# Kernel optimization log

Hardware: AMD Instinct MI355X
Metric: run time of the kernel (lower is better)

The kernel has to match this reference:

```python
import jax, jax.numpy as jnp
import numpy as np

D = 1024
H = 16
HD = D // H
SCALE = HD ** -0.5


def setup_inputs() -> dict:
    key = jax.random.key(0)
    ks = jax.random.split(key, 5)
    x = jax.random.normal(ks[0], (2, 2048, D), dtype=jnp.float32)
    s = 1.0 / np.sqrt(D)
    W_qkv = jax.random.uniform(ks[1], (D, 3 * D), jnp.float32, -s, s)
    b_qkv = jax.random.uniform(ks[2], (3 * D,), jnp.float32, -s, s)
    W_out = jax.random.uniform(ks[3], (D, D), jnp.float32, -s, s)
    b_out = jax.random.uniform(ks[4], (D,), jnp.float32, -s, s)
    return {"x": x, "W_qkv": W_qkv, "b_qkv": b_qkv, "W_out": W_out, "b_out": b_out}


def reference(x, W_qkv, b_qkv, W_out, b_out):
    B, S, _ = x.shape
    qkv = x @ W_qkv + b_qkv                       # [B,S,3D]
    qkv = qkv.reshape(B, S, 3, H, HD)
    q, k, v = jnp.moveaxis(qkv, 2, 0)             # each [B,S,H,HD]
    # scores: [B,H,S,S]
    scores = jnp.einsum("bshd,bthd->bhst", q, k) * SCALE
    attn = jax.nn.softmax(scores, axis=-1)        # dropout is identity in eval mode
    out = jnp.einsum("bhst,bthd->bshd", attn, v)  # [B,S,H,HD]
    out = out.reshape(B, S, H * HD)
    return out @ W_out + b_out
```

## Files before the change

### kernel.cpp

```cpp
#include <hip/hip_runtime.h>

typedef unsigned short u16;
typedef unsigned int   u32;

using short8 = __attribute__((ext_vector_type(8))) short;
using f32x4  = __attribute__((ext_vector_type(4))) float;
using half4  = __attribute__((ext_vector_type(4))) _Float16;
using half8  = __attribute__((ext_vector_type(8))) _Float16;

#define QSCALE 0.18033688011112042f

__device__ __forceinline__ u16 f2bf(float f) {
  u32 u = __float_as_uint(f);
  return (u16)((u + 0x8000u) >> 16);
}
__device__ __forceinline__ u16 f2h(float f) {
  _Float16 h = (_Float16)f;
  return __builtin_bit_cast(u16, h);
}

__device__ __forceinline__ void gld16(const u16* g, u16* l) {
  __builtin_amdgcn_global_load_lds(
      (const __attribute__((address_space(1))) unsigned int*)g,
      (__attribute__((address_space(3))) unsigned int*)l, 16, 0, 0);
}

__global__ __launch_bounds__(256) void cvt_x(const float* __restrict__ in,
                                             u16* __restrict__ out) {
  int idx = blockIdx.x * 256 + threadIdx.x;
  float4 v = reinterpret_cast<const float4*>(in)[idx];
  ushort4 o;
  o.x = f2bf(v.x); o.y = f2bf(v.y); o.z = f2bf(v.z); o.w = f2bf(v.w);
  reinterpret_cast<ushort4*>(out)[idx] = o;
}

__global__ __launch_bounds__(256) void transpose_w(const float* __restrict__ in,
                                                   u16* __restrict__ out,
                                                   int R, int C) {
  __shared__ u32 s[32][33];
  int c0 = blockIdx.x * 32, r0 = blockIdx.y * 32;
  int j = threadIdx.x & 31, i0 = threadIdx.x >> 5;
#pragma unroll
  for (int p = 0; p < 4; ++p) {
    int i = i0 + p * 8;
    s[i][j] = f2bf(in[(size_t)(r0 + i) * C + c0 + j]);
  }
  __syncthreads();
#pragma unroll
  for (int p = 0; p < 4; ++p) {
    int jj = i0 + p * 8;
    out[(size_t)(c0 + jj) * R + r0 + j] = (u16)s[j][jj];
  }
}

__global__ __launch_bounds__(256, 2) void gemm_qkv(
    const u16* __restrict__ A, const u16* __restrict__ Bt,
    const float* __restrict__ bias,
    u16* __restrict__ q_out, u16* __restrict__ k_out, u16* __restrict__ vt_out) {
  const int K = 1024;
  __shared__ __align__(16) u16 As[4][128 * 32];
  __shared__ __align__(16) u16 Bs[4][192 * 32];
  const int tid = threadIdx.x;
  const int lane = tid & 63, wv = tid >> 6;
  const int l16 = lane & 15, quad = lane >> 4;
  const int wm = wv & 1, wn = wv >> 1;
  const int bx = blockIdx.x, by = blockIdx.y;

  const u16* Ab = A + (size_t)by * 128 * K;
  const u16* Bb = Bt + (size_t)bx * 192 * K;

  const int iA0 = tid, iA1 = 256 + tid;
  const int iB0 = tid, iB1 = 256 + tid, iB2 = 512 + tid;
  const u16* sA0 = Ab + (size_t)(iA0 >> 2) * K + (((iA0 & 3) ^ ((iA0 >> 2) & 3)) << 3);
  const u16* sA1 = Ab + (size_t)(iA1 >> 2) * K + (((iA1 & 3) ^ ((iA1 >> 2) & 3)) << 3);
  const u16* sB0 = Bb + (size_t)(iB0 >> 2) * K + (((iB0 & 3) ^ ((iB0 >> 2) & 3)) << 3);
  const u16* sB1 = Bb + (size_t)(iB1 >> 2) * K + (((iB1 & 3) ^ ((iB1 >> 2) & 3)) << 3);
  const u16* sB2 = Bb + (size_t)(iB2 >> 2) * K + (((iB2 & 3) ^ ((iB2 >> 2) & 3)) << 3);
  const int dA0 = iA0 << 3, dA1 = iA1 << 3;
  const int dB0 = iB0 << 3, dB1 = iB1 << 3, dB2 = iB2 << 3;

  int aoff[4], boff[6];
#pragma unroll
  for (int mi = 0; mi < 4; ++mi) {
    int r = wm * 64 + mi * 16 + l16;
    aoff[mi] = r * 32 + ((quad ^ (r & 3)) << 3);
  }
#pragma unroll
  for (int ni = 0; ni < 6; ++ni) {
    int r = wn * 96 + ni * 16 + l16;
    boff[ni] = r * 32 + ((quad ^ (r & 3)) << 3);
  }

  const f32x4 fzero = {0.0f, 0.0f, 0.0f, 0.0f};
  f32x4 acc[4][6];
#pragma unroll
  for (int i = 0; i < 4; ++i)
#pragma unroll
    for (int j = 0; j < 6; ++j) acc[i][j] = fzero;

#define STAGE_A(T)                        \
  do {                                    \
    gld16(sA0, &As[T][dA0]);              \
    gld16(sA1, &As[T][dA1]);              \
    sA0 += 32; sA1 += 32;                 \
  } while (0)
#define STAGE_B(T)                        \
  do {                                    \
    gld16(sB0, &Bs[T][dB0]);              \
    gld16(sB1, &Bs[T][dB1]);              \
    gld16(sB2, &Bs[T][dB2]);              \
    sB0 += 32; sB1 += 32; sB2 += 32;      \
  } while (0)
#define VM5 asm volatile("s_waitcnt vmcnt(5)" ::: "memory")
#define VM0 asm volatile("s_waitcnt vmcnt(0)" ::: "memory")

#define GTILE(S, T, DOST, VW)                                              \
  do {                                                                     \
    short8 bb[6];                                                          \
    _Pragma("unroll")                                                      \
    for (int j = 0; j < 6; ++j)                                            \
      bb[j] = *reinterpret_cast<const short8*>(&Bs[S][boff[j]]);           \
    short8 a0 = *reinterpret_cast<const short8*>(&As[S][aoff[0]]);         \
    short8 a1 = *reinterpret_cast<const short8*>(&As[S][aoff[1]]);         \
    if (DOST) { STAGE_A(T); }                                              \
    __builtin_amdgcn_s_barrier();                                          \
    __builtin_amdgcn_s_setprio(1);                                         \
    _Pragma("unroll")                                                      \
    for (int j = 0; j < 6; ++j) {                                          \
      acc[0][j] = __builtin_amdgcn_mfma_f32_16x16x32_bf16(a0, bb[j], acc[0][j], 0, 0, 0); \
      acc[1][j] = __builtin_amdgcn_mfma_f32_16x16x32_bf16(a1, bb[j], acc[1][j], 0, 0, 0); \
    }                                                                      \
    __builtin_amdgcn_s_setprio(0);                                         \
    __builtin_amdgcn_s_barrier();                                          \
    short8 a2 = *reinterpret_cast<const short8*>(&As[S][aoff[2]]);         \
    short8 a3 = *reinterpret_cast<const short8*>(&As[S][aoff[3]]);         \
    if (DOST) { STAGE_B(T); }                                              \
    __builtin_amdgcn_s_barrier();                                          \
    __builtin_amdgcn_s_setprio(1);                                         \
    _Pragma("unroll")                                                      \
    for (int j = 0; j < 6; ++j) {                                          \
      acc[2][j] = __builtin_amdgcn_mfma_f32_16x16x32_bf16(a2, bb[j], acc[2][j], 0, 0, 0); \
      acc[3][j] = __builtin_amdgcn_mfma_f32_16x16x32_bf16(a3, bb[j], acc[3][j], 0, 0, 0); \
    }                                                                      \
    __builtin_amdgcn_s_setprio(0);                                         \
    VW;                                                                    \
    __builtin_amdgcn_s_barrier();                                          \
  } while (0)

  STAGE_A(0); STAGE_B(0);
  STAGE_A(1); STAGE_B(1);
  VM5;
  __builtin_amdgcn_s_barrier();

  for (int kb = 0; kb < 28; kb += 4) {
    GTILE(0, 2, 1, VM5);
    GTILE(1, 3, 1, VM5);
    GTILE(2, 0, 1, VM5);
    GTILE(3, 1, 1, VM5);
  }
  GTILE(0, 2, 1, VM5);
  GTILE(1, 3, 1, VM5);
  GTILE(2, 0, 0, VM0);
  GTILE(3, 1, 0, ((void)0));
#undef GTILE
#undef STAGE_A
#undef STAGE_B

#pragma unroll
  for (int mi = 0; mi < 4; ++mi)
#pragma unroll
    for (int ni = 0; ni < 6; ++ni) {
      int col = bx * 192 + wn * 96 + ni * 16 + l16;
      float bv = bias[col];
      int row0 = by * 128 + wm * 64 + mi * 16 + quad * 4;
      int which = col >> 10, rem = col & 1023;
      int h = rem >> 6, d = rem & 63;
      int b = row0 >> 11, sq0 = row0 & 2047;
      int bh = (b << 4) + h;
      if (which == 2) {
        ushort4 pk;
        pk.x = f2h(acc[mi][ni][0] + bv);
        pk.y = f2h(acc[mi][ni][1] + bv);
        pk.z = f2h(acc[mi][ni][2] + bv);
        pk.w = f2h(acc[mi][ni][3] + bv);
        size_t off = (size_t)bh * 131072 +
                     (((sq0 >> 2) * 16 + (d & 15)) * 16 + ((d >> 4) << 2));
        *reinterpret_cast<ushort4*>(&vt_out[off]) = pk;
      } else {
        size_t base = (size_t)(bh * 2048 + sq0) * 64 + d;
#pragma unroll
        for (int r = 0; r < 4; ++r) {
          float val = acc[mi][ni][r] + bv;
          if (which == 0) q_out[base + r * 64] = f2bf(val * QSCALE);
          else            k_out[base + r * 64] = f2bf(val);
        }
      }
    }
}

template <int EPI, int MT>
__global__ __launch_bounds__(256, 3) void gemm_bt(
    const u16* __restrict__ A, const u16* __restrict__ Bt,
    const float* __restrict__ bias, float* __restrict__ c_out,
    u16* __restrict__ q_out, u16* __restrict__ k_out, u16* __restrict__ vt_out,
    int M, int N, int K) {
  __shared__ __align__(16) u16 As[32 * MT * 32];
  __shared__ __align__(16) u16 Bs[128 * 32];
  const int tid = threadIdx.x;
  const int lane = tid & 63;
  const int wv = tid >> 6;
  const int l16 = lane & 15, quad = lane >> 4;
  const int wm = wv & 1, wn = wv >> 1;
  const int bx = blockIdx.x, by = blockIdx.y;

  const u16* Ab = A + (size_t)by * (32 * MT) * K;
  const u16* Bb = Bt + (size_t)bx * 128 * K;

  const f32x4 fzero = {0.0f, 0.0f, 0.0f, 0.0f};
  f32x4 acc[MT][4];
#pragma unroll
  for (int i = 0; i < MT; ++i)
#pragma unroll
    for (int j = 0; j < 4; ++j) acc[i][j] = fzero;

  for (int k0 = 0; k0 < K; k0 += 32) {
    __syncthreads();
#pragma unroll
    for (int p = 0; p < MT / 2; ++p) {
      int id = p * 256 + tid;
      int row = id >> 2, blk = id & 3;
      int gc = k0 + ((blk ^ (row & 3)) << 3);
      gld16(Ab + (size_t)row * K + gc, &As[id << 3]);
    }
#pragma unroll
    for (int p = 0; p < 2; ++p) {
      int id = p * 256 + tid;
      int row = id >> 2, blk = id & 3;
      int gc = k0 + ((blk ^ (row & 3)) << 3);
      gld16(Bb + (size_t)row * K + gc, &Bs[id << 3]);
    }
    __syncthreads();
    short8 af[MT], bfr[4];
#pragma unroll
    for (int mi = 0; mi < MT; ++mi) {
      int row = wm * (MT * 16) + mi * 16 + l16;
      af[mi] = *reinterpret_cast<const short8*>(&As[row * 32 + ((quad ^ (row & 3)) << 3)]);
    }
#pragma unroll
    for (int ni = 0; ni < 4; ++ni) {
      int row = wn * 64 + ni * 16 + l16;
      bfr[ni] = *reinterpret_cast<const short8*>(&Bs[row * 32 + ((quad ^ (row & 3)) << 3)]);
    }
#pragma unroll
    for (int mi = 0; mi < MT; ++mi)
#pragma unroll
      for (int ni = 0; ni < 4; ++ni)
        acc[mi][ni] = __builtin_amdgcn_mfma_f32_16x16x32_bf16(af[mi], bfr[ni], acc[mi][ni], 0, 0, 0);
  }

#pragma unroll
  for (int mi = 0; mi < MT; ++mi)
#pragma unroll
    for (int ni = 0; ni < 4; ++ni) {
      int col = bx * 128 + wn * 64 + ni * 16 + l16;
      float bv = bias[col];
      int row0 = by * (32 * MT) + wm * (MT * 16) + mi * 16 + quad * 4;
      if (EPI == 1) {
#pragma unroll
        for (int r = 0; r < 4; ++r)
          c_out[(size_t)(row0 + r) * N + col] = acc[mi][ni][r] + bv;
      } else {
        int which = col >> 10, rem = col & 1023;
        int h = rem >> 6, d = rem & 63;
        int b = row0 >> 11, sq0 = row0 & 2047;
        int bh = (b << 4) + h;
        if (which == 2) {
          ushort4 pk;
          pk.x = f2h(acc[mi][ni][0] + bv);
          pk.y = f2h(acc[mi][ni][1] + bv);
          pk.z = f2h(acc[mi][ni][2] + bv);
          pk.w = f2h(acc[mi][ni][3] + bv);
          size_t off = (size_t)bh * 131072 +
                       (((sq0 >> 2) * 16 + (d & 15)) * 16 + ((d >> 4) << 2));
          *reinterpret_cast<ushort4*>(&vt_out[off]) = pk;
        } else {
          size_t base = (size_t)(bh * 2048 + sq0) * 64 + d;
#pragma unroll
          for (int r = 0; r < 4; ++r) {
            float val = acc[mi][ni][r] + bv;
            if (which == 0) q_out[base + r * 64] = f2bf(val * QSCALE);
            else            k_out[base + r * 64] = f2bf(val);
          }
        }
      }
    }
}

__global__ __launch_bounds__(256, 4) void attn(
    const u16* __restrict__ q_buf, const u16* __restrict__ k_buf,
    const u16* __restrict__ vt_buf, u16* __restrict__ o_buf) {
  __shared__ __align__(16) u16 Ks[2][4096];
  __shared__ __align__(16) u16 Vs[2][4096];

  const int tid = threadIdx.x;
  const int lane = tid & 63, w = tid >> 6;
  const int l16 = lane & 15, quad = lane >> 4;
  const int bh = blockIdx.x, q0 = blockIdx.y * 64;

  const u16* qg = q_buf + (size_t)bh * 131072 + (q0 + w * 16) * 64;
  const u16* kg = k_buf + (size_t)bh * 131072;
  const u16* vg = vt_buf + (size_t)bh * 131072;

  short8 qb[2];
#pragma unroll
  for (int kk = 0; kk < 2; ++kk)
    qb[kk] = *reinterpret_cast<const short8*>(qg + l16 * 64 + kk * 32 + quad * 8);

  const int idA = tid, idB = 256 + tid;
  const u16* ksA = kg + (idA >> 3) * 64 + (((idA & 7) ^ ((idA >> 3) & 7)) << 3);
  const u16* ksB = kg + (idB >> 3) * 64 + (((idB & 7) ^ ((idB >> 3) & 7)) << 3);
  const u16* vsA = vg + ((idA ^ ((idA >> 4) & 1)) << 3);
  const u16* vsB = vg + ((idB ^ ((idB >> 4) & 1)) << 3);
  const int ldA = idA << 3, ldB = idB << 3;

  int k0o[4], k1o[4], v0o[4], v1o[4];
#pragma unroll
  for (int t = 0; t < 4; ++t) {
    int rr = t * 16 + l16;
    k0o[t] = rr * 64 + ((quad ^ (rr & 7)) << 3);
    k1o[t] = rr * 64 + (((4 + quad) ^ (rr & 7)) << 3);
    int gb = (t * 4 + quad) * 32 + l16 * 2;
    int sw = (l16 >> 3) & 1;
    v0o[t] = (gb + sw) << 3;
    v1o[t] = (gb + (sw ^ 1)) << 3;
  }

  const f32x4 fzero = {0.0f, 0.0f, 0.0f, 0.0f};
  f32x4 o_acc[4];
  float l_acc = 0.f;
#pragma unroll
  for (int nd = 0; nd < 4; ++nd) o_acc[nd] = fzero;

#define STAGE(BUF)                           \
  do {                                       \
    gld16(ksA, &Ks[BUF][ldA]);               \
    gld16(ksB, &Ks[BUF][ldB]);               \
    gld16(vsA, &Vs[BUF][ldA]);               \
    gld16(vsB, &Vs[BUF][ldB]);               \
    ksA += 4096; ksB += 4096;                \
    vsA += 4096; vsB += 4096;                \
  } while (0)

#define TILE(BUF)                                                         \
  do {                                                                    \
    _Pragma("unroll")                                                     \
    for (int t = 0; t < 4; ++t) {                                         \
      short8 k0f = *reinterpret_cast<const short8*>(&Ks[BUF][k0o[t]]);    \
      short8 k1f = *reinterpret_cast<const short8*>(&Ks[BUF][k1o[t]]);    \
      half8 v0 = *reinterpret_cast<const half8*>(&Vs[BUF][v0o[t]]);       \
      half8 v1 = *reinterpret_cast<const half8*>(&Vs[BUF][v1o[t]]);       \
      half4 vb0 = __builtin_shufflevector(v0, v0, 0, 1, 2, 3);            \
      half4 vb1 = __builtin_shufflevector(v0, v0, 4, 5, 6, 7);            \
      half4 vb2 = __builtin_shufflevector(v1, v1, 0, 1, 2, 3);            \
      half4 vb3 = __builtin_shufflevector(v1, v1, 4, 5, 6, 7);            \
      __builtin_amdgcn_s_setprio(1);                                      \
      f32x4 s = __builtin_amdgcn_mfma_f32_16x16x32_bf16(k0f, qb[0], fzero, 0, 0, 0); \
      s = __builtin_amdgcn_mfma_f32_16x16x32_bf16(k1f, qb[1], s, 0, 0, 0);\
      __builtin_amdgcn_s_setprio(0);                                      \
      float p0 = __builtin_amdgcn_exp2f(s[0]);                            \
      float p1 = __builtin_amdgcn_exp2f(s[1]);                            \
      float p2 = __builtin_amdgcn_exp2f(s[2]);                            \
      float p3 = __builtin_amdgcn_exp2f(s[3]);                            \
      l_acc += (p0 + p1) + (p2 + p3);                                     \
      half4 pa;                                                           \
      pa[0] = (_Float16)p0; pa[1] = (_Float16)p1;                         \
      pa[2] = (_Float16)p2; pa[3] = (_Float16)p3;                         \
      __builtin_amdgcn_s_setprio(1);                                      \
      o_acc[0] = __builtin_amdgcn_mfma_f32_16x16x16f16(pa, vb0, o_acc[0], 0, 0, 0); \
      o_acc[1] = __builtin_amdgcn_mfma_f32_16x16x16f16(pa, vb1, o_acc[1], 0, 0, 0); \
      o_acc[2] = __builtin_amdgcn_mfma_f32_16x16x16f16(pa, vb2, o_acc[2], 0, 0, 0); \
      o_acc[3] = __builtin_amdgcn_mfma_f32_16x16x16f16(pa, vb3, o_acc[3], 0, 0, 0); \
      __builtin_amdgcn_s_setprio(0);                                      \
    }                                                                     \
  } while (0)

  STAGE(0);
  __syncthreads();

  for (int i = 0; i < 32; i += 2) {
    if (i + 1 < 32) STAGE(1);
    TILE(0);
    __syncthreads();
    if (i + 2 < 32) STAGE(0);
    TILE(1);
    __syncthreads();
  }
#undef STAGE
#undef TILE

  l_acc += __shfl_xor(l_acc, 16, 64);
  l_acc += __shfl_xor(l_acc, 32, 64);

  const int b = bh >> 4, h = bh & 15;
  float lv[4];
#pragma unroll
  for (int r = 0; r < 4; ++r)
    lv[r] = __shfl(l_acc, quad * 4 + r, 64);
#pragma unroll
  for (int nd = 0; nd < 4; ++nd) {
#pragma unroll
    for (int r = 0; r < 4; ++r) {
      int sq = q0 + w * 16 + quad * 4 + r;
      o_buf[(size_t)(b * 2048 + sq) * 1024 + h * 64 + nd * 16 + l16] =
          f2bf(o_acc[nd][r] / lv[r]);
    }
  }
}

extern "C" void kernel_launch(void* const* d_in, const int* in_sizes, int n_in,
                              void* d_out, int out_size, void* d_ws, size_t ws_size,
                              hipStream_t stream) {
  (void)in_sizes; (void)n_in; (void)out_size; (void)ws_size;
  const float* x     = (const float*)d_in[0];
  const float* W_qkv = (const float*)d_in[1];
  const float* b_qkv = (const float*)d_in[2];
  const float* W_out = (const float*)d_in[3];
  const float* b_out = (const float*)d_in[4];
  float* out = (float*)d_out;

  char* ws = (char*)d_ws;
  u16* x_bf   = (u16*)(ws);
  u16* wqkv_t = (u16*)(ws + 8388608);
  u16* wout_t = (u16*)(ws + 14680064);
  u16* q_buf  = (u16*)(ws + 16777216);
  u16* k_buf  = (u16*)(ws + 25165824);
  u16* vt_buf = (u16*)(ws + 33554432);
  u16* o_bf   = (u16*)(ws + 41943040);

  cvt_x<<<4096, 256, 0, stream>>>(x, x_bf);
  transpose_w<<<dim3(96, 32), 256, 0, stream>>>(W_qkv, wqkv_t, 1024, 3072);
  transpose_w<<<dim3(32, 32), 256, 0, stream>>>(W_out, wout_t, 1024, 1024);
  gemm_qkv<<<dim3(16, 32), 256, 0, stream>>>(x_bf, wqkv_t, b_qkv,
                                             q_buf, k_buf, vt_buf);
  attn<<<dim3(32, 32), 256, 0, stream>>>(q_buf, k_buf, vt_buf, o_bf);
  gemm_bt<1, 2><<<dim3(8, 64), 256, 0, stream>>>(o_bf, wout_t, b_out, out,
                                                 nullptr, nullptr, nullptr, 4096, 1024, 1024);
}
```

Before: 188.3 us.

## Double per-wave query rows and use four-stage K/V pipeline in attention

Each wave in the attention kernel now handles 32 query rows instead of 16, so every K/V tile loaded into shared memory is reused for twice the MFMA work, and the grid is halved to match. K/V staging moves from a double buffer to a four-deep ring. Loads are issued inside the tile loop and waited on with explicit vmcnt counts and raw barriers in place of __syncthreads. The cost is more registers and LDS per block, and the launch bound drops occupancy from 4 to 2 blocks per CU, with half as many blocks to spread across CUs.

Measured after the change: 189.1 us. About the same (+0.4%).

```diff
diff --git a/kernel.cpp b/kernel.cpp
--- a/kernel.cpp
+++ b/kernel.cpp
@@ -296,25 +296,28 @@
     }
 }
 
-__global__ __launch_bounds__(256, 4) void attn(
+__global__ __launch_bounds__(256, 2) void attn(
     const u16* __restrict__ q_buf, const u16* __restrict__ k_buf,
     const u16* __restrict__ vt_buf, u16* __restrict__ o_buf) {
-  __shared__ __align__(16) u16 Ks[2][4096];
-  __shared__ __align__(16) u16 Vs[2][4096];
+  __shared__ __align__(16) u16 Ks[4][4096];
+  __shared__ __align__(16) u16 Vs[4][4096];
 
   const int tid = threadIdx.x;
   const int lane = tid & 63, w = tid >> 6;
   const int l16 = lane & 15, quad = lane >> 4;
-  const int bh = blockIdx.x, q0 = blockIdx.y * 64;
-
-  const u16* qg = q_buf + (size_t)bh * 131072 + (q0 + w * 16) * 64;
+  const int bh = blockIdx.x, q0 = blockIdx.y * 128;
+
+  const u16* qg = q_buf + (size_t)bh * 131072 + (q0 + w * 32) * 64;
   const u16* kg = k_buf + (size_t)bh * 131072;
   const u16* vg = vt_buf + (size_t)bh * 131072;
 
-  short8 qb[2];
-#pragma unroll
-  for (int kk = 0; kk < 2; ++kk)
-    qb[kk] = *reinterpret_cast<const short8*>(qg + l16 * 64 + kk * 32 + quad * 8);
+  short8 qb[2][2];
+#pragma unroll
+  for (int qi = 0; qi < 2; ++qi)
+#pragma unroll
+    for (int kk = 0; kk < 2; ++kk)
+      qb[qi][kk] = *reinterpret_cast<const short8*>(
+          qg + (qi * 16 + l16) * 64 + kk * 32 + quad * 8);
 
   const int idA = tid, idB = 256 + tid;
   const u16* ksA = kg + (idA >> 3) * 64 + (((idA & 7) ^ ((idA >> 3) & 7)) << 3);
@@ -336,83 +339,103 @@
   }
 
   const f32x4 fzero = {0.0f, 0.0f, 0.0f, 0.0f};
-  f32x4 o_acc[4];
-  float l_acc = 0.f;
-#pragma unroll
-  for (int nd = 0; nd < 4; ++nd) o_acc[nd] = fzero;
-
-#define STAGE(BUF)                           \
+  f32x4 o_acc[2][4];
+  float l_acc[2] = {0.f, 0.f};
+#pragma unroll
+  for (int qi = 0; qi < 2; ++qi)
+#pragma unroll
+    for (int nd = 0; nd < 4; ++nd) o_acc[qi][nd] = fzero;
+
+#define STAGE(T)                             \
   do {                                       \
-    gld16(ksA, &Ks[BUF][ldA]);               \
-    gld16(ksB, &Ks[BUF][ldB]);               \
-    gld16(vsA, &Vs[BUF][ldA]);               \
-    gld16(vsB, &Vs[BUF][ldB]);               \
+    gld16(ksA, &Ks[T][ldA]);                 \
+    gld16(ksB, &Ks[T][ldB]);                 \
+    gld16(vsA, &Vs[T][ldA]);                 \
+    gld16(vsB, &Vs[T][ldB]);                 \
     ksA += 4096; ksB += 4096;                \
     vsA += 4096; vsB += 4096;                \
   } while (0)
-
-#define TILE(BUF)                                                         \
+#define VM4 asm volatile("s_waitcnt vmcnt(4)" ::: "memory")
+#define VM0a asm volatile("s_waitcnt vmcnt(0)" ::: "memory")
+
+#define ATILE(S, T, DOST, VW)                                             \
   do {                                                                    \
     _Pragma("unroll")                                                     \
     for (int t = 0; t < 4; ++t) {                                         \
-      short8 k0f = *reinterpret_cast<const short8*>(&Ks[BUF][k0o[t]]);    \
-      short8 k1f = *reinterpret_cast<const short8*>(&Ks[BUF][k1o[t]]);    \
-      half8 v0 = *reinterpret_cast<const half8*>(&Vs[BUF][v0o[t]]);       \
-      half8 v1 = *reinterpret_cast<const half8*>(&Vs[BUF][v1o[t]]);       \
+      short8 k0f = *reinterpret_cast<const short8*>(&Ks[S][k0o[t]]);      \
+      short8 k1f = *reinterpret_cast<const short8*>(&Ks[S][k1o[t]]);      \
+      half8 v0 = *reinterpret_cast<const half8*>(&Vs[S][v0o[t]]);         \
+      half8 v1 = *reinterpret_cast<const half8*>(&Vs[S][v1o[t]]);         \
+      if (DOST && t == 0) STAGE(T);                                       \
       half4 vb0 = __builtin_shufflevector(v0, v0, 0, 1, 2, 3);            \
       half4 vb1 = __builtin_shufflevector(v0, v0, 4, 5, 6, 7);            \
       half4 vb2 = __builtin_shufflevector(v1, v1, 0, 1, 2, 3);            \
       half4 vb3 = __builtin_shufflevector(v1, v1, 4, 5, 6, 7);            \
-      __builtin_amdgcn_s_setprio(1);                                      \
-      f32x4 s = __builtin_amdgcn_mfma_f32_16x16x32_bf16(k0f, qb[0], fzero, 0, 0, 0); \
-      s = __builtin_amdgcn_mfma_f32_16x16x32_bf16(k1f, qb[1], s, 0, 0, 0);\
-      __builtin_amdgcn_s_setprio(0);                                      \
-      float p0 = __builtin_amdgcn_exp2f(s[0]);                            \
-      float p1 = __builtin_amdgcn_exp2f(s[1]);                            \
-      float p2 = __builtin_amdgcn_exp2f(s[2]);                            \
-      float p3 = __builtin_amdgcn_exp2f(s[3]);                            \
-      l_acc += (p0 + p1) + (p2 + p3);                                     \
-      half4 pa;                                                           \
-      pa[0] = (_Float16)p0; pa[1] = (_Float16)p1;                         \
-      pa[2] = (_Float16)p2; pa[3] = (_Float16)p3;                         \
-      __builtin_amdgcn_s_setprio(1);                                      \
-      o_acc[0] = __builtin_amdgcn_mfma_f32_16x16x16f16(pa, vb0, o_acc[0], 0, 0, 0); \
-      o_acc[1] = __builtin_amdgcn_mfma_f32_16x16x16f16(pa, vb1, o_acc[1], 0, 0, 0); \
-      o_acc[2] = __builtin_amdgcn_mfma_f32_16x16x16f16(pa, vb2, o_acc[2], 0, 0, 0); \
-      o_acc[3] = __builtin_amdgcn_mfma_f32_16x16x16f16(pa, vb3, o_acc[3], 0, 0, 0); \
-      __builtin_amdgcn_s_setprio(0);                                      \
+      _Pragma("unroll")                                                   \
+      for (int qi = 0; qi < 2; ++qi) {                                    \
+        __builtin_amdgcn_s_setprio(1);                                    \
+        f32x4 s = __builtin_amdgcn_mfma_f32_16x16x32_bf16(k0f, qb[qi][0], fzero, 0, 0, 0); \
+        s = __builtin_amdgcn_mfma_f32_16x16x32_bf16(k1f, qb[qi][1], s, 0, 0, 0); \
+        __builtin_amdgcn_s_setprio(0);                                    \
+        float p0 = __builtin_amdgcn_exp2f(s[0]);                          \
+        float p1 = __builtin_amdgcn_exp2f(s[1]);                          \
+        float p2 = __builtin_amdgcn_exp2f(s[2]);                          \
+        float p3 = __builtin_amdgcn_exp2f(s[3]);                          \
+        l_acc[qi] += (p0 + p1) + (p2 + p3);                               \
+        half4 pa;                                                         \
+        pa[0] = (_Float16)p0; pa[1] = (_Float16)p1;                       \
+        pa[2] = (_Float16)p2; pa[3] = (_Float16)p3;                       \
+        __builtin_amdgcn_s_setprio(1);                                    \
+        o_acc[qi][0] = __builtin_amdgcn_mfma_f32_16x16x16f16(pa, vb0, o_acc[qi][0], 0, 0, 0); \
+        o_acc[qi][1] = __builtin_amdgcn_mfma_f32_16x16x16f16(pa, vb1, o_acc[qi][1], 0, 0, 0); \
+        o_acc[qi][2] = __builtin_amdgcn_mfma_f32_16x16x16f16(pa, vb2, o_acc[qi][2], 0, 0, 0); \
+        o_acc[qi][3] = __builtin_amdgcn_mfma_f32_16x16x16f16(pa, vb3, o_acc[qi][3], 0, 0, 0); \
+        __builtin_amdgcn_s_setprio(0);                                    \
+      }                                                                   \
     }                                                                     \
+    VW;                                                                   \
+    __builtin_amdgcn_s_barrier();                                         \
   } while (0)
 
   STAGE(0);
-  __syncthreads();
-
-  for (int i = 0; i < 32; i += 2) {
-    if (i + 1 < 32) STAGE(1);
-    TILE(0);
-    __syncthreads();
-    if (i + 2 < 32) STAGE(0);
-    TILE(1);
-    __syncthreads();
-  }
+  STAGE(1);
+  VM4;
+  __builtin_amdgcn_s_barrier();
+
+  for (int i = 0; i < 28; i += 4) {
+    ATILE(0, 2, 1, VM4);
+    ATILE(1, 3, 1, VM4);
+    ATILE(2, 0, 1, VM4);
+    ATILE(3, 1, 1, VM4);
+  }
+  ATILE(0, 2, 1, VM4);
+  ATILE(1, 3, 1, VM4);
+  ATILE(2, 0, 0, VM0a);
+  ATILE(3, 0, 0, ((void)0));
+#undef ATILE
 #undef STAGE
-#undef TILE
-
-  l_acc += __shfl_xor(l_acc, 16, 64);
-  l_acc += __shfl_xor(l_acc, 32, 64);
+
+#pragma unroll
+  for (int qi = 0; qi < 2; ++qi) {
+    l_acc[qi] += __shfl_xor(l_acc[qi], 16, 64);
+    l_acc[qi] += __shfl_xor(l_acc[qi], 32, 64);
+  }
 
   const int b = bh >> 4, h = bh & 15;
-  float lv[4];
-#pragma unroll
-  for (int r = 0; r < 4; ++r)
-    lv[r] = __shfl(l_acc, quad * 4 + r, 64);
-#pragma unroll
-  for (int nd = 0; nd < 4; ++nd) {
-#pragma unroll
-    for (int r = 0; r < 4; ++r) {
-      int sq = q0 + w * 16 + quad * 4 + r;
-      o_buf[(size_t)(b * 2048 + sq) * 1024 + h * 64 + nd * 16 + l16] =
-          f2bf(o_acc[nd][r] / lv[r]);
+#pragma unroll
+  for (int qi = 0; qi < 2; ++qi) {
+    float lv[4];
+#pragma unroll
+    for (int r = 0; r < 4; ++r)
+      lv[r] = __shfl(l_acc[qi], quad * 4 + r, 64);
+#pragma unroll
+    for (int nd = 0; nd < 4; ++nd) {
+#pragma unroll
+      for (int r = 0; r < 4; ++r) {
+        int sq = q0 + w * 32 + qi * 16 + quad * 4 + r;
+        o_buf[(size_t)(b * 2048 + sq) * 1024 + h * 64 + nd * 16 + l16] =
+            f2bf(o_acc[qi][nd][r] / lv[r]);
+      }
     }
   }
 }
@@ -442,7 +465,7 @@
   transpose_w<<<dim3(32, 32), 256, 0, stream>>>(W_out, wout_t, 1024, 1024);
   gemm_qkv<<<dim3(16, 32), 256, 0, stream>>>(x_bf, wqkv_t, b_qkv,
                                              q_buf, k_buf, vt_buf);
-  attn<<<dim3(32, 32), 256, 0, stream>>>(q_buf, k_buf, vt_buf, o_bf);
+  attn<<<dim3(32, 16), 256, 0, stream>>>(q_buf, k_buf, vt_buf, o_bf);
   gemm_bt<1, 2><<<dim3(8, 64), 256, 0, stream>>>(o_bf, wout_t, b_out, out,
                                                  nullptr, nullptr, nullptr, 4096, 1024, 1024);
 }
```

## Merge prep kernels and pipeline output projection GEMM with 4-stage async loads

Applied to the files above, without the earlier changes.

Folds the x conversion and both weight transposes into one prep kernel, which removes two launches. Replaces the output-projection GEMM's single-buffered loop with a 4-stage global_load_lds pipeline modelled on the QKV GEMM, with interleaved barriers, setprio and partial vmcnt waits, on 128x64 tiles. It also changes the LDS XOR swizzle to mix in higher row bits, which is meant to reduce bank conflicts. The cost is more LDS per block and occupancy dropping from 3 to 2 blocks.

Result: faster. 184.3 us (-2.1%).

```diff
diff --git a/kernel.cpp b/kernel.cpp
--- a/kernel.cpp
+++ b/kernel.cpp
@@ -9,6 +9,7 @@
 using half8  = __attribute__((ext_vector_type(8))) _Float16;
 
 #define QSCALE 0.18033688011112042f
+#define SXR(r) ((((r) ^ ((r) >> 2))) & 3)
 
 __device__ __forceinline__ u16 f2bf(float f) {
   u32 u = __float_as_uint(f);
@@ -25,21 +26,25 @@
       (__attribute__((address_space(3))) unsigned int*)l, 16, 0, 0);
 }
 
-__global__ __launch_bounds__(256) void cvt_x(const float* __restrict__ in,
-                                             u16* __restrict__ out) {
-  int idx = blockIdx.x * 256 + threadIdx.x;
-  float4 v = reinterpret_cast<const float4*>(in)[idx];
-  ushort4 o;
-  o.x = f2bf(v.x); o.y = f2bf(v.y); o.z = f2bf(v.z); o.w = f2bf(v.w);
-  reinterpret_cast<ushort4*>(out)[idx] = o;
-}
-
-__global__ __launch_bounds__(256) void transpose_w(const float* __restrict__ in,
-                                                   u16* __restrict__ out,
-                                                   int R, int C) {
+__global__ __launch_bounds__(256) void prep(
+    const float* __restrict__ x, u16* __restrict__ x_bf,
+    const float* __restrict__ Wq, u16* __restrict__ wq_t,
+    const float* __restrict__ Wo, u16* __restrict__ wo_t) {
   __shared__ u32 s[32][33];
-  int c0 = blockIdx.x * 32, r0 = blockIdx.y * 32;
-  int j = threadIdx.x & 31, i0 = threadIdx.x >> 5;
+  const int bid = blockIdx.x, tid = threadIdx.x;
+  if (bid < 4096) {
+    int idx = bid * 256 + tid;
+    float4 v = reinterpret_cast<const float4*>(x)[idx];
+    ushort4 o;
+    o.x = f2bf(v.x); o.y = f2bf(v.y); o.z = f2bf(v.z); o.w = f2bf(v.w);
+    reinterpret_cast<ushort4*>(x_bf)[idx] = o;
+    return;
+  }
+  const float* in; u16* out; int R, C, bx, by;
+  if (bid < 7168) { int b = bid - 4096; in = Wq; out = wq_t; R = 1024; C = 3072; bx = b % 96; by = b / 96; }
+  else            { int b = bid - 7168; in = Wo; out = wo_t; R = 1024; C = 1024; bx = b % 32; by = b / 32; }
+  int c0 = bx * 32, r0 = by * 32;
+  int j = tid & 31, i0 = tid >> 5;
 #pragma unroll
   for (int p = 0; p < 4; ++p) {
     int i = i0 + p * 8;
@@ -71,11 +76,11 @@
 
   const int iA0 = tid, iA1 = 256 + tid;
   const int iB0 = tid, iB1 = 256 + tid, iB2 = 512 + tid;
-  const u16* sA0 = Ab + (size_t)(iA0 >> 2) * K + (((iA0 & 3) ^ ((iA0 >> 2) & 3)) << 3);
-  const u16* sA1 = Ab + (size_t)(iA1 >> 2) * K + (((iA1 & 3) ^ ((iA1 >> 2) & 3)) << 3);
-  const u16* sB0 = Bb + (size_t)(iB0 >> 2) * K + (((iB0 & 3) ^ ((iB0 >> 2) & 3)) << 3);
-  const u16* sB1 = Bb + (size_t)(iB1 >> 2) * K + (((iB1 & 3) ^ ((iB1 >> 2) & 3)) << 3);
-  const u16* sB2 = Bb + (size_t)(iB2 >> 2) * K + (((iB2 & 3) ^ ((iB2 >> 2) & 3)) << 3);
+  const u16* sA0 = Ab + (size_t)(iA0 >> 2) * K + (((iA0 & 3) ^ SXR(iA0 >> 2)) << 3);
+  const u16* sA1 = Ab + (size_t)(iA1 >> 2) * K + (((iA1 & 3) ^ SXR(iA1 >> 2)) << 3);
+  const u16* sB0 = Bb + (size_t)(iB0 >> 2) * K + (((iB0 & 3) ^ SXR(iB0 >> 2)) << 3);
+  const u16* sB1 = Bb + (size_t)(iB1 >> 2) * K + (((iB1 & 3) ^ SXR(iB1 >> 2)) << 3);
+  const u16* sB2 = Bb + (size_t)(iB2 >> 2) * K + (((iB2 & 3) ^ SXR(iB2 >> 2)) << 3);
   const int dA0 = iA0 << 3, dA1 = iA1 << 3;
   const int dB0 = iB0 << 3, dB1 = iB1 << 3, dB2 = iB2 << 3;
 
@@ -83,12 +88,12 @@
 #pragma unroll
   for (int mi = 0; mi < 4; ++mi) {
     int r = wm * 64 + mi * 16 + l16;
-    aoff[mi] = r * 32 + ((quad ^ (r & 3)) << 3);
+    aoff[mi] = r * 32 + ((quad ^ SXR(r)) << 3);
   }
 #pragma unroll
   for (int ni = 0; ni < 6; ++ni) {
     int r = wn * 96 + ni * 16 + l16;
-    boff[ni] = r * 32 + ((quad ^ (r & 3)) << 3);
+    boff[ni] = r * 32 + ((quad ^ SXR(r)) << 3);
   }
 
   const f32x4 fzero = {0.0f, 0.0f, 0.0f, 0.0f};
@@ -198,101 +203,118 @@
     }
 }
 
-template <int EPI, int MT>
-__global__ __launch_bounds__(256, 3) void gemm_bt(
+__global__ __launch_bounds__(256, 2) void gemm_op(
     const u16* __restrict__ A, const u16* __restrict__ Bt,
-    const float* __restrict__ bias, float* __restrict__ c_out,
-    u16* __restrict__ q_out, u16* __restrict__ k_out, u16* __restrict__ vt_out,
-    int M, int N, int K) {
-  __shared__ __align__(16) u16 As[32 * MT * 32];
-  __shared__ __align__(16) u16 Bs[128 * 32];
+    const float* __restrict__ bias, float* __restrict__ c_out) {
+  const int K = 1024;
+  __shared__ __align__(16) u16 As[4][128 * 32];
+  __shared__ __align__(16) u16 Bs[4][64 * 32];
   const int tid = threadIdx.x;
-  const int lane = tid & 63;
-  const int wv = tid >> 6;
+  const int lane = tid & 63, wv = tid >> 6;
   const int l16 = lane & 15, quad = lane >> 4;
   const int wm = wv & 1, wn = wv >> 1;
   const int bx = blockIdx.x, by = blockIdx.y;
 
-  const u16* Ab = A + (size_t)by * (32 * MT) * K;
-  const u16* Bb = Bt + (size_t)bx * 128 * K;
+  const u16* Ab = A + (size_t)by * 128 * K;
+  const u16* Bb = Bt + (size_t)bx * 64 * K;
+
+  const int iA0 = tid, iA1 = 256 + tid, iB0 = tid;
+  const u16* sA0 = Ab + (size_t)(iA0 >> 2) * K + (((iA0 & 3) ^ SXR(iA0 >> 2)) << 3);
+  const u16* sA1 = Ab + (size_t)(iA1 >> 2) * K + (((iA1 & 3) ^ SXR(iA1 >> 2)) << 3);
+  const u16* sB0 = Bb + (size_t)(iB0 >> 2) * K + (((iB0 & 3) ^ SXR(iB0 >> 2)) << 3);
+  const int dA0 = iA0 << 3, dA1 = iA1 << 3, dB0 = iB0 << 3;
+
+  int aoff[4], boff[2];
+#pragma unroll
+  for (int mi = 0; mi < 4; ++mi) {
+    int r = wm * 64 + mi * 16 + l16;
+    aoff[mi] = r * 32 + ((quad ^ SXR(r)) << 3);
+  }
+#pragma unroll
+  for (int ni = 0; ni < 2; ++ni) {
+    int r = wn * 32 + ni * 16 + l16;
+    boff[ni] = r * 32 + ((quad ^ SXR(r)) << 3);
+  }
 
   const f32x4 fzero = {0.0f, 0.0f, 0.0f, 0.0f};
-  f32x4 acc[MT][4];
-#pragma unroll
-  for (int i = 0; i < MT; ++i)
-#pragma unroll
-    for (int j = 0; j < 4; ++j) acc[i][j] = fzero;
-
-  for (int k0 = 0; k0 < K; k0 += 32) {
-    __syncthreads();
-#pragma unroll
-    for (int p = 0; p < MT / 2; ++p) {
-      int id = p * 256 + tid;
-      int row = id >> 2, blk = id & 3;
-      int gc = k0 + ((blk ^ (row & 3)) << 3);
-      gld16(Ab + (size_t)row * K + gc, &As[id << 3]);
-    }
-#pragma unroll
-    for (int p = 0; p < 2; ++p) {
-      int id = p * 256 + tid;
-      int row = id >> 2, blk = id & 3;
-      int gc = k0 + ((blk ^ (row & 3)) << 3);
-      gld16(Bb + (size_t)row * K + gc, &Bs[id << 3]);
-    }
-    __syncthreads();
-    short8 af[MT], bfr[4];
-#pragma unroll
-    for (int mi = 0; mi < MT; ++mi) {
-      int row = wm * (MT * 16) + mi * 16 + l16;
-      af[mi] = *reinterpret_cast<const short8*>(&As[row * 32 + ((quad ^ (row & 3)) << 3)]);
-    }
-#pragma unroll
-    for (int ni = 0; ni < 4; ++ni) {
-      int row = wn * 64 + ni * 16 + l16;
-      bfr[ni] = *reinterpret_cast<const short8*>(&Bs[row * 32 + ((quad ^ (row & 3)) << 3)]);
-    }
-#pragma unroll
-    for (int mi = 0; mi < MT; ++mi)
-#pragma unroll
-      for (int ni = 0; ni < 4; ++ni)
-        acc[mi][ni] = __builtin_amdgcn_mfma_f32_16x16x32_bf16(af[mi], bfr[ni], acc[mi][ni], 0, 0, 0);
-  }
-
-#pragma unroll
-  for (int mi = 0; mi < MT; ++mi)
-#pragma unroll
-    for (int ni = 0; ni < 4; ++ni) {
-      int col = bx * 128 + wn * 64 + ni * 16 + l16;
+  f32x4 acc[4][2];
+#pragma unroll
+  for (int i = 0; i < 4; ++i)
+#pragma unroll
+    for (int j = 0; j < 2; ++j) acc[i][j] = fzero;
+
+#define STAGE_A(T)                        \
+  do {                                    \
+    gld16(sA0, &As[T][dA0]);              \
+    gld16(sA1, &As[T][dA1]);              \
+    sA0 += 32; sA1 += 32;                 \
+  } while (0)
+#define STAGE_B(T)                        \
+  do {                                    \
+    gld16(sB0, &Bs[T][dB0]);              \
+    sB0 += 32;                            \
+  } while (0)
+#define VM3 asm volatile("s_waitcnt vmcnt(3)" ::: "memory")
+#define VM0b asm volatile("s_waitcnt vmcnt(0)" ::: "memory")
+
+#define OTILE(S, T, DOST, VW)                                              \
+  do {                                                                     \
+    short8 b0 = *reinterpret_cast<const short8*>(&Bs[S][boff[0]]);         \
+    short8 b1 = *reinterpret_cast<const short8*>(&Bs[S][boff[1]]);         \
+    short8 a0 = *reinterpret_cast<const short8*>(&As[S][aoff[0]]);         \
+    short8 a1 = *reinterpret_cast<const short8*>(&As[S][aoff[1]]);         \
+    if (DOST) { STAGE_A(T); }                                              \
+    __builtin_amdgcn_s_barrier();                                          \
+    __builtin_amdgcn_s_setprio(1);                                         \
+    acc[0][0] = __builtin_amdgcn_mfma_f32_16x16x32_bf16(a0, b0, acc[0][0], 0, 0, 0); \
+    acc[0][1] = __builtin_amdgcn_mfma_f32_16x16x32_bf16(a0, b1, acc[0][1], 0, 0, 0); \
+    acc[1][0] = __builtin_amdgcn_mfma_f32_16x16x32_bf16(a1, b0, acc[1][0], 0, 0, 0); \
+    acc[1][1] = __builtin_amdgcn_mfma_f32_16x16x32_bf16(a1, b1, acc[1][1], 0, 0, 0); \
+    __builtin_amdgcn_s_setprio(0);                                         \
+    __builtin_amdgcn_s_barrier();                                          \
+    short8 a2 = *reinterpret_cast<const short8*>(&As[S][aoff[2]]);         \
+    short8 a3 = *reinterpret_cast<const short8*>(&As[S][aoff[3]]);         \
+    if (DOST) { STAGE_B(T); }                                              \
+    __builtin_amdgcn_s_barrier();                                          \
+    __builtin_amdgcn_s_setprio(1);                                         \
+    acc[2][0] = __builtin_amdgcn_mfma_f32_16x16x32_bf16(a2, b0, acc[2][0], 0, 0, 0); \
+    acc[2][1] = __builtin_amdgcn_mfma_f32_16x16x32_bf16(a2, b1, acc[2][1], 0, 0, 0); \
+    acc[3][0] = __builtin_amdgcn_mfma_f32_16x16x32_bf16(a3, b0, acc[3][0], 0, 0, 0); \
+    acc[3][1] = __builtin_amdgcn_mfma_f32_16x16x32_bf16(a3, b1, acc[3][1], 0, 0, 0); \
+    __builtin_amdgcn_s_setprio(0);                                         \
+    VW;                                                                    \
+    __builtin_amdgcn_s_barrier();                                          \
+  } while (0)
+
+  STAGE_A(0); STAGE_B(0);
+  STAGE_A(1); STAGE_B(1);
+  VM3;
+  __builtin_amdgcn_s_barrier();
+
+  for (int kb = 0; kb < 28; kb += 4) {
+    OTILE(0, 2, 1, VM3);
+    OTILE(1, 3, 1, VM3);
+    OTILE(2, 0, 1, VM3);
+    OTILE(3, 1, 1, VM3);
+  }
+  OTILE(0, 2, 1, VM3);
+  OTILE(1, 3, 1, VM3);
+  OTILE(2, 0, 0, VM0b);
+  OTILE(3, 1, 0, ((void)0));
+#undef OTILE
+#undef STAGE_A
+#undef STAGE_B
+
+#pragma unroll
+  for (int mi = 0; mi < 4; ++mi)
+#pragma unroll
+    for (int ni = 0; ni < 2; ++ni) {
+      int col = bx * 64 + wn * 32 + ni * 16 + l16;
       float bv = bias[col];
-      int row0 = by * (32 * MT) + wm * (MT * 16) + mi * 16 + quad * 4;
-      if (EPI == 1) {
-#pragma unroll
-        for (int r = 0; r < 4; ++r)
-          c_out[(size_t)(row0 + r) * N + col] = acc[mi][ni][r] + bv;
-      } else {
-        int which = col >> 10, rem = col & 1023;
-        int h = rem >> 6, d = rem & 63;
-        int b = row0 >> 11, sq0 = row0 & 2047;
-        int bh = (b << 4) + h;
-        if (which == 2) {
-          ushort4 pk;
-          pk.x = f2h(acc[mi][ni][0] + bv);
-          pk.y = f2h(acc[mi][ni][1] + bv);
-          pk.z = f2h(acc[mi][ni][2] + bv);
-          pk.w = f2h(acc[mi][ni][3] + bv);
-          size_t off = (size_t)bh * 131072 +
-                       (((sq0 >> 2) * 16 + (d & 15)) * 16 + ((d >> 4) << 2));
-          *reinterpret_cast<ushort4*>(&vt_out[off]) = pk;
-        } else {
-          size_t base = (size_t)(bh * 2048 + sq0) * 64 + d;
-#pragma unroll
-          for (int r = 0; r < 4; ++r) {
-            float val = acc[mi][ni][r] + bv;
-            if (which == 0) q_out[base + r * 64] = f2bf(val * QSCALE);
-            else            k_out[base + r * 64] = f2bf(val);
-          }
-        }
-      }
+      int row0 = by * 128 + wm * 64 + mi * 16 + quad * 4;
+#pragma unroll
+      for (int r = 0; r < 4; ++r)
+        c_out[(size_t)(row0 + r) * 1024 + col] = acc[mi][ni][r] + bv;
     }
 }
 
@@ -437,12 +459,9 @@
   u16* vt_buf = (u16*)(ws + 33554432);
   u16* o_bf   = (u16*)(ws + 41943040);
 
-  cvt_x<<<4096, 256, 0, stream>>>(x, x_bf);
-  transpose_w<<<dim3(96, 32), 256, 0, stream>>>(W_qkv, wqkv_t, 1024, 3072);
-  transpose_w<<<dim3(32, 32), 256, 0, stream>>>(W_out, wout_t, 1024, 1024);
+  prep<<<8192, 256, 0, stream>>>(x, x_bf, W_qkv, wqkv_t, W_out, wout_t);
   gemm_qkv<<<dim3(16, 32), 256, 0, stream>>>(x_bf, wqkv_t, b_qkv,
                                              q_buf, k_buf, vt_buf);
   attn<<<dim3(32, 32), 256, 0, stream>>>(q_buf, k_buf, vt_buf, o_bf);
-  gemm_bt<1, 2><<<dim3(8, 64), 256, 0, stream>>>(o_bf, wout_t, b_out, out,
-                                                 nullptr, nullptr, nullptr, 4096, 1024, 1024);
-}
+  gemm_op<<<dim3(16, 32), 256, 0, stream>>>(o_bf, wout_t, b_out, out);
+}
```
